# Performance work log

Measured on AMD Instinct MI355X. Metric: run time of the kernel, lower is better.

## Reference

```python
import jax, jax.numpy as jnp
import numpy as np

SEQ, BATCH = 128, 256
INPUT_BITS, STATE_BITS = 256, 256
N_IN, N_ST = 1024, 256        # n_state_neurons == state_size_bits (recurrence constraint)
NB_IN, NB_ST = 16, 16         # bits per neuron -> RAM size 2**16 per neuron


def setup_inputs() -> dict:
    key = jax.random.key(0)
    k1, k2, k3, k4, k5, k6 = jax.random.split(key, 6)
    input_seq_bits = jax.random.randint(k1, (SEQ, BATCH, INPUT_BITS), 0, 2).astype(bool)
    init_state = jax.random.randint(k2, (BATCH, STATE_BITS), 0, 2).astype(bool)
    # random bit connections: input layer reads from input_bits+state_bits (512),
    # state layer reads from input_layer_out+state_bits (1280)
    input_conn = jax.random.randint(k3, (N_IN, NB_IN), 0, INPUT_BITS + STATE_BITS)
    state_conn = jax.random.randint(k5, (N_ST, NB_ST), 0, N_IN + STATE_BITS)
    # per-neuron RAM contents (bool words)
    input_mem = jax.random.randint(k4, (N_IN, 2 ** NB_IN), 0, 2).astype(bool)
    state_mem = jax.random.randint(k6, (N_ST, 2 ** NB_ST), 0, 2).astype(bool)
    return {
        "input_seq_bits": input_seq_bits,
        "init_state": init_state,
        "input_conn": input_conn,
        "input_mem": input_mem,
        "state_conn": state_conn,
        "state_mem": state_mem,
    }


def _ram(bits, conn, mem):
    # bits: [B, T_bits] bool; conn: [N, nb] int; mem: [N, 2**nb]
    sel = bits[:, conn].astype(jnp.int32)                 # [B, N, nb]
    w = (1 << jnp.arange(conn.shape[1], dtype=jnp.int32))  # bit k -> 2**k
    addr = jnp.sum(sel * w, axis=-1)                      # [B, N]
    return mem[jnp.arange(mem.shape[0])[None, :], addr]   # [B, N]


def reference(input_seq_bits, init_state, input_conn, input_mem, state_conn, state_mem):
    def step(state, inp):
        # input_layer: [input_bits | prev_state]
        io = _ram(jnp.concatenate([inp, state], axis=1), input_conn, input_mem)
        # state_layer: [input_layer_out | prev_state]
        ns = _ram(jnp.concatenate([io, state], axis=1), state_conn, state_mem)
        return ns, io

    final_state, outs = jax.lax.scan(step, init_state, input_seq_bits)
    return outs, final_state  # [SEQ, BATCH, N_IN] bool, [BATCH, N_ST] bool
```

## Files before the change

### kernel.cpp

```cpp
#include <hip/hip_runtime.h>
#include <stdint.h>

#define SEQ 128
#define BATCH 256
#define INPUT_BITS 256
#define STATE_BITS 256
#define N_IN 1024
#define N_ST 256
#define NB 16
#define RAM_WORDS 2048

typedef uint32_t u32x4 __attribute__((ext_vector_type(4)));

__global__ __launch_bounds__(256)
void pack_bits_kernel(const u32x4* __restrict__ src, uint32_t* __restrict__ dst) {
    int i = blockIdx.x * blockDim.x + threadIdx.x;
    const u32x4* p = src + (size_t)i * 8;
    uint32_t w = 0;
#pragma unroll
    for (int j = 0; j < 8; j++) {
        u32x4 v = __builtin_nontemporal_load(p + j);
        w |= (v.x != 0u ? 1u : 0u) << (4 * j + 0);
        w |= (v.y != 0u ? 1u : 0u) << (4 * j + 1);
        w |= (v.z != 0u ? 1u : 0u) << (4 * j + 2);
        w |= (v.w != 0u ? 1u : 0u) << (4 * j + 3);
    }
    dst[i] = w;
}

__global__ __launch_bounds__(1024)
void ram_automaton_kernel(
    const uint32_t* __restrict__ seq_bits,
    const uint32_t* __restrict__ init_state,
    const int*      __restrict__ input_conn,
    const int*      __restrict__ state_conn,
    const uint32_t* __restrict__ pim,
    const uint32_t* __restrict__ psm,
    const uint32_t* __restrict__ im_raw,
    const uint32_t* __restrict__ sm_raw,
    int* __restrict__ outs,
    int* __restrict__ final_state,
    int packed)
{
    __shared__ uint32_t c0[16];
    __shared__ uint32_t c1[40];

    const int b = blockIdx.x;
    const int tid = threadIdx.x;
    const int lane = tid & 63;

    int ic[NB];
#pragma unroll
    for (int k = 0; k < NB; k++) ic[k] = input_conn[tid * NB + k];
    int sc[NB];
    if (tid < N_ST) {
#pragma unroll
        for (int k = 0; k < NB; k++) sc[k] = state_conn[tid * NB + k];
    }

    uint32_t nsbit = 0;
    if (tid < N_ST) nsbit = (init_state[(size_t)b * STATE_BITS + tid] != 0u) ? 1u : 0u;

    uint32_t inbit = 0;
    if (tid < INPUT_BITS) inbit = seq_bits[((size_t)0 * BATCH + b) * INPUT_BITS + tid];

    for (int t = 0; t < SEQ; t++) {
        if (tid < INPUT_BITS) {
            uint64_t mi = __ballot(inbit != 0u);
            uint64_t ms = __ballot(nsbit != 0u);
            if ((lane & 31) == 0) {
                c0[tid >> 5] = (uint32_t)(mi >> (lane & 32));
                uint32_t ws = (uint32_t)(ms >> (lane & 32));
                c0[8 + (tid >> 5)]  = ws;
                c1[32 + (tid >> 5)] = ws;
            }
        }
        __syncthreads();

        if (t + 1 < SEQ && tid < INPUT_BITS) {
            inbit = __builtin_nontemporal_load(
                seq_bits + ((size_t)(t + 1) * BATCH + b) * INPUT_BITS + tid);
        }

        {
            int addr = 0;
#pragma unroll
            for (int k = 0; k < NB; k++) {
                int c = ic[k];
                uint32_t w = c0[c >> 5];
                addr |= (int)((w >> (c & 31)) & 1u) << k;
            }
            uint32_t bit;
            if (packed) {
                uint32_t w = pim[(tid << 11) + (addr >> 5)];
                bit = (w >> (addr & 31)) & 1u;
            } else {
                bit = (im_raw[((size_t)tid << 16) + (size_t)addr] != 0u) ? 1u : 0u;
            }
            __builtin_nontemporal_store((int)bit,
                outs + ((size_t)t * BATCH + b) * N_IN + tid);
            uint64_t m = __ballot(bit != 0u);
            if (lane == 0) {
                c1[(tid >> 5)]     = (uint32_t)m;
                c1[(tid >> 5) + 1] = (uint32_t)(m >> 32);
            }
        }
        __syncthreads();

        if (tid < N_ST) {
            int addr = 0;
#pragma unroll
            for (int k = 0; k < NB; k++) {
                int c = sc[k];
                uint32_t w = c1[c >> 5];
                addr |= (int)((w >> (c & 31)) & 1u) << k;
            }
            if (packed) {
                uint32_t w = psm[(tid << 11) + (addr >> 5)];
                nsbit = (w >> (addr & 31)) & 1u;
            } else {
                nsbit = (sm_raw[((size_t)tid << 16) + (size_t)addr] != 0u) ? 1u : 0u;
            }
        }
        __syncthreads();
    }

    if (tid < N_ST) {
        final_state[(size_t)b * N_ST + tid] = (int)nsbit;
    }
}

extern "C" void kernel_launch(void* const* d_in, const int* in_sizes, int n_in,
                              void* d_out, int out_size, void* d_ws, size_t ws_size,
                              hipStream_t stream) {
    const uint32_t* seq        = (const uint32_t*)d_in[0];
    const uint32_t* init_state = (const uint32_t*)d_in[1];
    const int*      input_conn = (const int*)d_in[2];
    const uint32_t* input_mem  = (const uint32_t*)d_in[3];
    const int*      state_conn = (const int*)d_in[4];
    const uint32_t* state_mem  = (const uint32_t*)d_in[5];

    int* outs = (int*)d_out;
    int* fin  = outs + (size_t)SEQ * BATCH * N_IN;

    const size_t pim_words = (size_t)N_IN * RAM_WORDS;
    const size_t psm_words = (size_t)N_ST * RAM_WORDS;
    const size_t need = (pim_words + psm_words) * sizeof(uint32_t);

    uint32_t* pim = nullptr;
    uint32_t* psm = nullptr;
    int packed = 0;
    if (ws_size >= need) {
        packed = 1;
        pim = (uint32_t*)d_ws;
        psm = pim + pim_words;
        hipLaunchKernelGGL(pack_bits_kernel,
                           dim3((unsigned)(pim_words / 256)), dim3(256), 0, stream,
                           (const u32x4*)input_mem, pim);
        hipLaunchKernelGGL(pack_bits_kernel,
                           dim3((unsigned)(psm_words / 256)), dim3(256), 0, stream,
                           (const u32x4*)state_mem, psm);
    }

    hipLaunchKernelGGL(ram_automaton_kernel, dim3(BATCH), dim3(1024), 0, stream,
                       seq, init_state, input_conn, state_conn,
                       pim, psm, input_mem, state_mem, outs, fin, packed);
}
```

Before: 946.1 us.

## Split input-layer neurons across blocks with cross-block spin exchange per step

Replaces the one-block-per-batch-row kernel with 256 blocks of 8 waves. Each block owns one 128-neuron slice of the input layer for 8 batch rows, and every slice redundantly computes the full state layer. Input-layer results travel between the 8 slice blocks through tagged atomic words in global memory, polled with spin-waits. Input sequence and initial state are pre-packed to bits, and the per-wave flow needs no block-wide barriers. The risk is a deadlock if the co-dependent blocks are not all resident at once (a bounded guard is included), plus spin-polling latency on every time step.

```diff
diff --git a/kernel.cpp b/kernel.cpp
--- a/kernel.cpp
+++ b/kernel.cpp
@@ -10,6 +10,7 @@
 #define NB 16
 #define RAM_WORDS 2048
 
+typedef unsigned long long u64;
 typedef uint32_t u32x4 __attribute__((ext_vector_type(4)));
 
 __global__ __launch_bounds__(256)
@@ -28,27 +29,155 @@
     dst[i] = w;
 }
 
-__global__ __launch_bounds__(1024)
-void ram_automaton_kernel(
-    const uint32_t* __restrict__ seq_bits,
-    const uint32_t* __restrict__ init_state,
+__global__ __launch_bounds__(512)
+void ram_sliced_kernel(
+    const uint32_t* __restrict__ pseq,
+    const uint32_t* __restrict__ pinit,
     const int*      __restrict__ input_conn,
     const int*      __restrict__ state_conn,
     const uint32_t* __restrict__ pim,
     const uint32_t* __restrict__ psm,
-    const uint32_t* __restrict__ im_raw,
-    const uint32_t* __restrict__ sm_raw,
-    int* __restrict__ outs,
-    int* __restrict__ final_state,
-    int packed)
+    u64*            __restrict__ ex,
+    int*            __restrict__ outs,
+    int*            __restrict__ final_state)
+{
+    __shared__ uint32_t ctx[8 * 48];
+
+    const int tid  = threadIdx.x;
+    const int lane = tid & 63;
+    const int w    = tid >> 6;
+    const int s    = blockIdx.x & 7;
+    const int j    = blockIdx.x >> 3;
+    const int gb   = j * 8 + w;
+    const int base = w * 48;
+
+    uint32_t icr[2][16];
+#pragma unroll
+    for (int m = 0; m < 2; m++) {
+        int n = s * 128 + lane + 64 * m;
+#pragma unroll
+        for (int k = 0; k < 16; k++) {
+            int c = input_conn[n * 16 + k];
+            int sel = (c < 256) ? (c >> 5) : (8 + ((c - 256) >> 5));
+            icr[m][k] = ((uint32_t)(base + sel) << 8) | (uint32_t)(c & 31);
+        }
+    }
+    uint32_t scr[4][16];
+#pragma unroll
+    for (int m = 0; m < 4; m++) {
+        int n = lane + 64 * m;
+#pragma unroll
+        for (int k = 0; k < 16; k++) {
+            int c = state_conn[n * 16 + k];
+            int sel = (c < 1024) ? (16 + (c >> 5)) : (8 + ((c - 1024) >> 5));
+            scr[m][k] = ((uint32_t)(base + sel) << 8) | (uint32_t)(c & 31);
+        }
+    }
+
+    if (lane < 8) ctx[base + 8 + lane] = pinit[gb * 8 + lane];
+    uint32_t sreg = 0;
+    if (lane < 8) sreg = pseq[(size_t)gb * 8 + lane];
+
+    uint32_t sb0 = 0, sb1 = 0, sb2 = 0, sb3 = 0;
+
+    for (int t = 0; t < SEQ; t++) {
+        const u64 tag = (u64)(t + 1);
+
+        if (lane < 8) ctx[base + lane] = sreg;
+        if (t + 1 < SEQ && lane < 8)
+            sreg = pseq[((size_t)(t + 1) * BATCH + gb) * 8 + lane];
+
+        uint32_t bit0, bit1;
+        {
+            uint32_t a0 = 0, a1 = 0;
+#pragma unroll
+            for (int k = 0; k < 16; k++) {
+                uint32_t r0 = icr[0][k], r1 = icr[1][k];
+                a0 |= ((ctx[r0 >> 8] >> (r0 & 31)) & 1u) << k;
+                a1 |= ((ctx[r1 >> 8] >> (r1 & 31)) & 1u) << k;
+            }
+            int n0 = s * 128 + lane, n1 = n0 + 64;
+            uint32_t t0 = pim[((size_t)n0 << 11) + (a0 >> 5)];
+            uint32_t t1 = pim[((size_t)n1 << 11) + (a1 >> 5)];
+            bit0 = (t0 >> (a0 & 31)) & 1u;
+            bit1 = (t1 >> (a1 & 31)) & 1u;
+            int* op = outs + ((size_t)t * BATCH + gb) * N_IN + n0;
+            __builtin_nontemporal_store((int)bit0, op);
+            __builtin_nontemporal_store((int)bit1, op + 64);
+        }
+        u64 m0 = __ballot(bit0 != 0u);
+        u64 m1 = __ballot(bit1 != 0u);
+
+        if (lane < 4) {
+            uint32_t half = (lane < 2) ? (uint32_t)(m0 >> (lane * 32))
+                                       : (uint32_t)(m1 >> ((lane - 2) * 32));
+            u64 v = ((tag << 16) | (half & 0xFFFFu))
+                  | ((((tag << 16) | (half >> 16))) << 32);
+            __hip_atomic_store(&ex[(((size_t)(t & 1) * BATCH) + gb) * 32 + s * 4 + lane],
+                               v, __ATOMIC_RELAXED, __HIP_MEMORY_SCOPE_AGENT);
+        }
+
+        if (lane < 32) {
+            const u64* p = &ex[(((size_t)(t & 1) * BATCH) + gb) * 32 + lane];
+            u64 v; int guard = 0;
+            for (;;) {
+                v = __hip_atomic_load(p, __ATOMIC_RELAXED, __HIP_MEMORY_SCOPE_AGENT);
+                if ((((v >> 16) & 0xFFFFull) == tag) && ((v >> 48) == tag)) break;
+                if (++guard > (1 << 22)) break;
+                __builtin_amdgcn_s_sleep(1);
+            }
+            ctx[base + 16 + lane] =
+                (uint32_t)(v & 0xFFFFu) | (((uint32_t)(v >> 32) & 0xFFFFu) << 16);
+        }
+
+        {
+            uint32_t a0 = 0, a1 = 0, a2 = 0, a3 = 0;
+#pragma unroll
+            for (int k = 0; k < 16; k++) {
+                uint32_t r0 = scr[0][k], r1 = scr[1][k], r2 = scr[2][k], r3 = scr[3][k];
+                a0 |= ((ctx[r0 >> 8] >> (r0 & 31)) & 1u) << k;
+                a1 |= ((ctx[r1 >> 8] >> (r1 & 31)) & 1u) << k;
+                a2 |= ((ctx[r2 >> 8] >> (r2 & 31)) & 1u) << k;
+                a3 |= ((ctx[r3 >> 8] >> (r3 & 31)) & 1u) << k;
+            }
+            uint32_t t0 = psm[((size_t)(lane      ) << 11) + (a0 >> 5)];
+            uint32_t t1 = psm[((size_t)(lane +  64) << 11) + (a1 >> 5)];
+            uint32_t t2 = psm[((size_t)(lane + 128) << 11) + (a2 >> 5)];
+            uint32_t t3 = psm[((size_t)(lane + 192) << 11) + (a3 >> 5)];
+            sb0 = (t0 >> (a0 & 31)) & 1u;
+            sb1 = (t1 >> (a1 & 31)) & 1u;
+            sb2 = (t2 >> (a2 & 31)) & 1u;
+            sb3 = (t3 >> (a3 & 31)) & 1u;
+        }
+        u64 q0 = __ballot(sb0 != 0u);
+        u64 q1 = __ballot(sb1 != 0u);
+        u64 q2 = __ballot(sb2 != 0u);
+        u64 q3 = __ballot(sb3 != 0u);
+        if (lane < 8) {
+            int mi = lane >> 1;
+            u64 qq = (mi == 0) ? q0 : (mi == 1) ? q1 : (mi == 2) ? q2 : q3;
+            ctx[base + 8 + lane] = (uint32_t)(qq >> ((lane & 1) * 32));
+        }
+    }
+
+    if (s == 0) {
+        final_state[(size_t)gb * N_ST + lane +   0] = (int)sb0;
+        final_state[(size_t)gb * N_ST + lane +  64] = (int)sb1;
+        final_state[(size_t)gb * N_ST + lane + 128] = (int)sb2;
+        final_state[(size_t)gb * N_ST + lane + 192] = (int)sb3;
+    }
+}
+
+__global__ __launch_bounds__(1024)
+void ram_automaton_fallback(
+    const uint32_t* __restrict__ seq_bits, const uint32_t* __restrict__ init_state,
+    const int* __restrict__ input_conn, const int* __restrict__ state_conn,
+    const uint32_t* __restrict__ im_raw, const uint32_t* __restrict__ sm_raw,
+    int* __restrict__ outs, int* __restrict__ final_state)
 {
     __shared__ uint32_t c0[16];
     __shared__ uint32_t c1[40];
-
-    const int b = blockIdx.x;
-    const int tid = threadIdx.x;
-    const int lane = tid & 63;
-
+    const int b = blockIdx.x, tid = threadIdx.x, lane = tid & 63;
     int ic[NB];
 #pragma unroll
     for (int k = 0; k < NB; k++) ic[k] = input_conn[tid * NB + k];
@@ -57,77 +186,48 @@
 #pragma unroll
         for (int k = 0; k < NB; k++) sc[k] = state_conn[tid * NB + k];
     }
-
     uint32_t nsbit = 0;
     if (tid < N_ST) nsbit = (init_state[(size_t)b * STATE_BITS + tid] != 0u) ? 1u : 0u;
-
     uint32_t inbit = 0;
-    if (tid < INPUT_BITS) inbit = seq_bits[((size_t)0 * BATCH + b) * INPUT_BITS + tid];
-
+    if (tid < INPUT_BITS) inbit = seq_bits[(size_t)b * INPUT_BITS + tid];
     for (int t = 0; t < SEQ; t++) {
         if (tid < INPUT_BITS) {
-            uint64_t mi = __ballot(inbit != 0u);
-            uint64_t ms = __ballot(nsbit != 0u);
+            u64 mi = __ballot(inbit != 0u);
+            u64 ms = __ballot(nsbit != 0u);
             if ((lane & 31) == 0) {
                 c0[tid >> 5] = (uint32_t)(mi >> (lane & 32));
-                uint32_t ws = (uint32_t)(ms >> (lane & 32));
-                c0[8 + (tid >> 5)]  = ws;
-                c1[32 + (tid >> 5)] = ws;
+                uint32_t wsd = (uint32_t)(ms >> (lane & 32));
+                c0[8 + (tid >> 5)] = wsd; c1[32 + (tid >> 5)] = wsd;
             }
         }
         __syncthreads();
-
-        if (t + 1 < SEQ && tid < INPUT_BITS) {
-            inbit = __builtin_nontemporal_load(
-                seq_bits + ((size_t)(t + 1) * BATCH + b) * INPUT_BITS + tid);
-        }
-
+        if (t + 1 < SEQ && tid < INPUT_BITS)
+            inbit = seq_bits[((size_t)(t + 1) * BATCH + b) * INPUT_BITS + tid];
         {
             int addr = 0;
 #pragma unroll
             for (int k = 0; k < NB; k++) {
                 int c = ic[k];
-                uint32_t w = c0[c >> 5];
-                addr |= (int)((w >> (c & 31)) & 1u) << k;
-            }
-            uint32_t bit;
-            if (packed) {
-                uint32_t w = pim[(tid << 11) + (addr >> 5)];
-                bit = (w >> (addr & 31)) & 1u;
-            } else {
-                bit = (im_raw[((size_t)tid << 16) + (size_t)addr] != 0u) ? 1u : 0u;
-            }
-            __builtin_nontemporal_store((int)bit,
-                outs + ((size_t)t * BATCH + b) * N_IN + tid);
-            uint64_t m = __ballot(bit != 0u);
-            if (lane == 0) {
-                c1[(tid >> 5)]     = (uint32_t)m;
-                c1[(tid >> 5) + 1] = (uint32_t)(m >> 32);
-            }
+                addr |= (int)((c0[c >> 5] >> (c & 31)) & 1u) << k;
+            }
+            uint32_t bit = (im_raw[((size_t)tid << 16) + (size_t)addr] != 0u) ? 1u : 0u;
+            __builtin_nontemporal_store((int)bit, outs + ((size_t)t * BATCH + b) * N_IN + tid);
+            u64 m = __ballot(bit != 0u);
+            if (lane == 0) { c1[tid >> 5] = (uint32_t)m; c1[(tid >> 5) + 1] = (uint32_t)(m >> 32); }
         }
         __syncthreads();
-
         if (tid < N_ST) {
             int addr = 0;
 #pragma unroll
             for (int k = 0; k < NB; k++) {
                 int c = sc[k];
-                uint32_t w = c1[c >> 5];
-                addr |= (int)((w >> (c & 31)) & 1u) << k;
-            }
-            if (packed) {
-                uint32_t w = psm[(tid << 11) + (addr >> 5)];
-                nsbit = (w >> (addr & 31)) & 1u;
-            } else {
-                nsbit = (sm_raw[((size_t)tid << 16) + (size_t)addr] != 0u) ? 1u : 0u;
-            }
+                addr |= (int)((c1[c >> 5] >> (c & 31)) & 1u) << k;
+            }
+            nsbit = (sm_raw[((size_t)tid << 16) + (size_t)addr] != 0u) ? 1u : 0u;
         }
         __syncthreads();
     }
-
-    if (tid < N_ST) {
-        final_state[(size_t)b * N_ST + tid] = (int)nsbit;
-    }
+    if (tid < N_ST) final_state[(size_t)b * N_ST + tid] = (int)nsbit;
 }
 
 extern "C" void kernel_launch(void* const* d_in, const int* in_sizes, int n_in,
@@ -143,26 +243,36 @@
     int* outs = (int*)d_out;
     int* fin  = outs + (size_t)SEQ * BATCH * N_IN;
 
+    const size_t ex_u64    = (size_t)2 * BATCH * 32;
     const size_t pim_words = (size_t)N_IN * RAM_WORDS;
     const size_t psm_words = (size_t)N_ST * RAM_WORDS;
-    const size_t need = (pim_words + psm_words) * sizeof(uint32_t);
-
-    uint32_t* pim = nullptr;
-    uint32_t* psm = nullptr;
-    int packed = 0;
+    const size_t pseq_words = (size_t)SEQ * BATCH * 8;
+    const size_t pinit_words = (size_t)BATCH * 8;
+    const size_t need = ex_u64 * 8 +
+        (pim_words + psm_words + pseq_words + pinit_words) * 4;
+
     if (ws_size >= need) {
-        packed = 1;
-        pim = (uint32_t*)d_ws;
-        psm = pim + pim_words;
-        hipLaunchKernelGGL(pack_bits_kernel,
-                           dim3((unsigned)(pim_words / 256)), dim3(256), 0, stream,
-                           (const u32x4*)input_mem, pim);
-        hipLaunchKernelGGL(pack_bits_kernel,
-                           dim3((unsigned)(psm_words / 256)), dim3(256), 0, stream,
-                           (const u32x4*)state_mem, psm);
-    }
-
-    hipLaunchKernelGGL(ram_automaton_kernel, dim3(BATCH), dim3(1024), 0, stream,
-                       seq, init_state, input_conn, state_conn,
-                       pim, psm, input_mem, state_mem, outs, fin, packed);
-}
+        u64*      ex    = (u64*)d_ws;
+        uint32_t* pim   = (uint32_t*)(ex + ex_u64);
+        uint32_t* psm   = pim + pim_words;
+        uint32_t* pseq  = psm + psm_words;
+        uint32_t* pinit = pseq + pseq_words;
+
+        hipLaunchKernelGGL(pack_bits_kernel, dim3((unsigned)(pim_words / 256)),
+                           dim3(256), 0, stream, (const u32x4*)input_mem, pim);
+        hipLaunchKernelGGL(pack_bits_kernel, dim3((unsigned)(psm_words / 256)),
+                           dim3(256), 0, stream, (const u32x4*)state_mem, psm);
+        hipLaunchKernelGGL(pack_bits_kernel, dim3((unsigned)(pseq_words / 256)),
+                           dim3(256), 0, stream, (const u32x4*)seq, pseq);
+        hipLaunchKernelGGL(pack_bits_kernel, dim3((unsigned)(pinit_words / 256)),
+                           dim3(256), 0, stream, (const u32x4*)init_state, pinit);
+
+        hipLaunchKernelGGL(ram_sliced_kernel, dim3(BATCH), dim3(512), 0, stream,
+                           pseq, pinit, input_conn, state_conn, pim, psm,
+                           ex, outs, fin);
+    } else {
+        hipLaunchKernelGGL(ram_automaton_fallback, dim3(BATCH), dim3(1024), 0, stream,
+                           seq, init_state, input_conn, state_conn,
+                           input_mem, state_mem, outs, fin);
+    }
+}
```

After: 1.272 ms. 34.4% more time.
